# Performance work log

Measured on AMD Instinct MI355X. Metric: run time of the kernel, lower is better.

Reference implementation:

```python
import jax, jax.numpy as jnp
import numpy as np

B, N, C, K, OUT = 4, 10000, 128, 16, 128


def setup_inputs() -> dict:
    key = jax.random.key(0)
    k1, k2, k3, k4 = jax.random.split(key, 4)
    x = jax.random.normal(k1, (B, N, C), dtype=jnp.float32)
    edge_index = jax.random.randint(k2, (2, B, N, K), 0, N)
    # Linear(2C -> OUT), torch convention W: [OUT, 2C]
    W = jax.random.normal(k3, (OUT, 2 * C), dtype=jnp.float32) * 0.05
    b = jax.random.normal(k4, (OUT,), dtype=jnp.float32) * 0.05
    return {"x": x, "edge_index": edge_index, "W": W, "b": b}


def reference(x, edge_index, W, b):
    # x: [B, N, C] -> [B, C, N]
    xt = jnp.swapaxes(x, 1, 2)
    Bs, Cs, Ns = xt.shape
    # batched_index_select: [C, N] gathered by [N, K] -> [C, N, K], vmapped over batch
    gather = jax.vmap(lambda xb, ib: xb[:, ib])
    x_i = gather(xt, edge_index[1])  # [B, C, N, K]
    x_j = gather(xt, edge_index[0])  # [B, C, N, K]
    rel = jnp.max(x_j - x_i, axis=-1)  # max-relative: [B, C, N]
    # interleave channels: [x_0, rel_0, x_1, rel_1, ...] -> [B, 2C, N]
    feat = jnp.stack([xt, rel], axis=2).reshape(Bs, 2 * Cs, Ns)
    feat = jnp.swapaxes(feat, 1, 2)  # [B, N, 2C]
    out = feat @ W.T + b  # Linear(2C -> OUT)
    return jax.nn.relu(out)
```

## Files before the change

### kernel.cpp

```cpp
#include <hip/hip_runtime.h>


#define Bn 4
#define Nn 10000
#define Cn 128
#define Kn 16
#define OUTn 128
#define Mn 16
#define FPAD 8

typedef __attribute__((ext_vector_type(8))) short short8;
typedef __attribute__((ext_vector_type(4))) float floatx4;

__device__ __forceinline__ unsigned short f2bf(float f) {
    union { float f; unsigned u; } v; v.f = f;
    unsigned r = v.u + 0x7fffu + ((v.u >> 16) & 1u);
    return (unsigned short)(r >> 16);
}
__device__ __forceinline__ float bf2f(unsigned short h) {
    union { unsigned u; float f; } v; v.u = ((unsigned)h) << 16;
    return v.f;
}

__global__ __launch_bounds__(256) void prep_kernel(const float* __restrict__ x,
                                                   const float* __restrict__ W,
                                                   unsigned short* __restrict__ xh,
                                                   unsigned short* __restrict__ Wb) {
    int bi = blockIdx.x;
    int t = threadIdx.x;
    if (bi < 16) {
        int tid = bi * 256 + t;
        int lane = tid & 63;
        int step = (tid >> 6) & 7;
        int tile = tid >> 9;
        int o = tile * 16 + (lane & 15);
        int quad = lane >> 4;
        unsigned short v[8];
#pragma unroll
        for (int j = 0; j < 8; ++j) {
            int c2 = step * 32 + quad * 8 + j;
            v[j] = f2bf(W[o * (2 * Cn) + c2]);
        }
        uint4 pk;
        pk.x = (unsigned)v[0] | ((unsigned)v[1] << 16);
        pk.y = (unsigned)v[2] | ((unsigned)v[3] << 16);
        pk.z = (unsigned)v[4] | ((unsigned)v[5] << 16);
        pk.w = (unsigned)v[6] | ((unsigned)v[7] << 16);
        *(uint4*)(Wb + (size_t)tid * 8) = pk;
        return;
    }
    int i = (bi - 16) * 256 + t;
    const float4* x4 = (const float4*)x;
    float4 a = x4[2 * i];
    float4 c = x4[2 * i + 1];
    uint4 pk;
    pk.x = (unsigned)f2bf(a.x) | ((unsigned)f2bf(a.y) << 16);
    pk.y = (unsigned)f2bf(a.z) | ((unsigned)f2bf(a.w) << 16);
    pk.z = (unsigned)f2bf(c.x) | ((unsigned)f2bf(c.y) << 16);
    pk.w = (unsigned)f2bf(c.z) | ((unsigned)f2bf(c.w) << 16);
    *(uint4*)(xh + 8 * (size_t)i) = pk;
}

__global__ __launch_bounds__(256) void mrconv_batch(
    const unsigned short* __restrict__ xh, const int* __restrict__ edge,
    const unsigned short* __restrict__ Wb, const float* __restrict__ bias,
    float* __restrict__ out, int b)
{
    __shared__ unsigned short sfeat[Mn][2 * Cn + FPAD];
    __shared__ int sidx[2][Mn][Kn];

    const int nb = blockIdx.x;
    const int n0 = nb * Mn;
    const int gbase = b * Nn + n0;

    const int t = threadIdx.x;
    const int wv = t >> 6;
    const int lane = t & 63;

    for (int i = t; i < 2 * Mn * Kn; i += 256) {
        int s = i >> 8;
        int m = (i >> 4) & 15;
        int k = i & 15;
        sidx[s][m][k] = __builtin_nontemporal_load(
            &edge[s * (Bn * Nn * Kn) + (gbase + m) * Kn + k]);
    }
    __syncthreads();

    const unsigned short* xbb = xh + (size_t)b * Nn * Cn;

    {
        const int q = lane >> 4;
        const int l16 = lane & 15;
        const int m = wv * 4 + q;
        const int ch = l16 * 8;
        const short8 xs = *(const short8*)(xbb + (n0 + m) * Cn + ch);
        float r[8];
#pragma unroll
        for (int e = 0; e < 8; ++e) r[e] = -3.402823466e+38f;
#pragma unroll
        for (int kc = 0; kc < 2; ++kc) {
            short8 vj[8], vi[8];
#pragma unroll
            for (int u = 0; u < 8; ++u) {
                const int jj = sidx[0][m][kc * 8 + u];
                const int ii = sidx[1][m][kc * 8 + u];
                vj[u] = *(const short8*)(xbb + jj * Cn + ch);
                vi[u] = *(const short8*)(xbb + ii * Cn + ch);
            }
#pragma unroll
            for (int u = 0; u < 8; ++u) {
#pragma unroll
                for (int e = 0; e < 8; ++e) {
                    r[e] = fmaxf(r[e], bf2f((unsigned short)vj[u][e]) -
                                       bf2f((unsigned short)vi[u][e]));
                }
            }
        }
        uint4 pk0, pk1;
        pk0.x = (unsigned short)xs[0] | ((unsigned)f2bf(r[0]) << 16);
        pk0.y = (unsigned short)xs[1] | ((unsigned)f2bf(r[1]) << 16);
        pk0.z = (unsigned short)xs[2] | ((unsigned)f2bf(r[2]) << 16);
        pk0.w = (unsigned short)xs[3] | ((unsigned)f2bf(r[3]) << 16);
        pk1.x = (unsigned short)xs[4] | ((unsigned)f2bf(r[4]) << 16);
        pk1.y = (unsigned short)xs[5] | ((unsigned)f2bf(r[5]) << 16);
        pk1.z = (unsigned short)xs[6] | ((unsigned)f2bf(r[6]) << 16);
        pk1.w = (unsigned short)xs[7] | ((unsigned)f2bf(r[7]) << 16);
        *(uint4*)&sfeat[m][2 * ch] = pk0;
        *(uint4*)&sfeat[m][2 * ch + 8] = pk1;
    }
    __syncthreads();

    const int m16 = lane & 15;
    const int quad = lane >> 4;
    floatx4 acc0 = {0.f, 0.f, 0.f, 0.f};
    floatx4 acc1 = {0.f, 0.f, 0.f, 0.f};
    const short8* wb8 = (const short8*)Wb;
    const int tile0 = 2 * wv, tile1 = 2 * wv + 1;
#pragma unroll
    for (int step = 0; step < 8; ++step) {
        short8 a = *(const short8*)&sfeat[m16][step * 32 + quad * 8];
        short8 b0 = wb8[(tile0 * 8 + step) * 64 + lane];
        short8 b1 = wb8[(tile1 * 8 + step) * 64 + lane];
        acc0 = __builtin_amdgcn_mfma_f32_16x16x32_bf16(a, b0, acc0, 0, 0, 0);
        acc1 = __builtin_amdgcn_mfma_f32_16x16x32_bf16(a, b1, acc1, 0, 0, 0);
    }
    const int o0 = tile0 * 16 + m16;
    const int o1 = tile1 * 16 + m16;
    const float bb0 = bias[o0], bb1 = bias[o1];
#pragma unroll
    for (int r = 0; r < 4; ++r) {
        int g = gbase + quad * 4 + r;
        __builtin_nontemporal_store(fmaxf(acc0[r] + bb0, 0.f), &out[g * OUTn + o0]);
        __builtin_nontemporal_store(fmaxf(acc1[r] + bb1, 0.f), &out[g * OUTn + o1]);
    }
}

extern "C" void kernel_launch(void* const* d_in, const int* in_sizes, int n_in,
                              void* d_out, int out_size, void* d_ws, size_t ws_size,
                              hipStream_t stream) {
    const float* x = (const float*)d_in[0];
    const int* edge = (const int*)d_in[1];
    const float* W = (const float*)d_in[2];
    const float* bias = (const float*)d_in[3];
    float* out = (float*)d_out;

    unsigned short* Wb = (unsigned short*)d_ws;
    unsigned short* xh = (unsigned short*)((char*)d_ws + 65536);

    prep_kernel<<<2516, 256, 0, stream>>>(x, W, xh, Wb);
    for (int b = 0; b < Bn; ++b) {
        mrconv_batch<<<Nn / Mn, 256, 0, stream>>>(xh, edge, Wb, bias, out, b);
    }
}
```

Baseline: 114.8 us.

## Merge per-batch launches into one kernel with XCD-affine dynamic tile scheduling

Replaces four per-batch launches with a single launch whose blocks read their XCC id, pick a batch from it, and claim tiles through atomic counters, stealing from other batches once their own runs out. The aim is to keep each batch's gathered bf16 x rows inside one XCD's L2 for better gather hit rates, and to remove launch gaps and tail effects between batches. It adds a global atomic per block and an inline s_getreg of HW_REG_XCC_ID, and relies on the counters being zeroed by the prep kernel. The grid is 2560 blocks, which exactly covers the 2500 tiles plus a few spares that exit early.

```diff
diff --git a/kernel.cpp b/kernel.cpp
--- a/kernel.cpp
+++ b/kernel.cpp
@@ -7,6 +7,7 @@
 #define Kn 16
 #define OUTn 128
 #define Mn 16
+#define NT (Nn / Mn)
 #define FPAD 8
 
 typedef __attribute__((ext_vector_type(8))) short short8;
@@ -25,10 +26,12 @@
 __global__ __launch_bounds__(256) void prep_kernel(const float* __restrict__ x,
                                                    const float* __restrict__ W,
                                                    unsigned short* __restrict__ xh,
-                                                   unsigned short* __restrict__ Wb) {
+                                                   unsigned short* __restrict__ Wb,
+                                                   int* __restrict__ cnt) {
     int bi = blockIdx.x;
     int t = threadIdx.x;
     if (bi < 16) {
+        if (bi == 0 && t < 8) cnt[t] = 0;
         int tid = bi * 256 + t;
         int lane = tid & 63;
         int step = (tid >> 6) & 7;
@@ -61,19 +64,39 @@
     *(uint4*)(xh + 8 * (size_t)i) = pk;
 }
 
-__global__ __launch_bounds__(256) void mrconv_batch(
+__global__ __launch_bounds__(256) void mrconv_kernel(
     const unsigned short* __restrict__ xh, const int* __restrict__ edge,
     const unsigned short* __restrict__ Wb, const float* __restrict__ bias,
-    float* __restrict__ out, int b)
+    float* __restrict__ out, int* __restrict__ cnt)
 {
     __shared__ unsigned short sfeat[Mn][2 * Cn + FPAD];
     __shared__ int sidx[2][Mn][Kn];
+    __shared__ int s_hdr[2];
 
-    const int nb = blockIdx.x;
+    const int t = threadIdx.x;
+
+    if (t == 0) {
+        unsigned xcc = 0;
+        asm volatile("s_getreg_b32 %0, hwreg(HW_REG_XCC_ID)" : "=s"(xcc));
+        int b = (int)(xcc & 3u);
+        int tile = atomicAdd(&cnt[b], 1);
+        int tries = 0;
+        while (tile >= NT && tries < 3) {
+            b = (b + 1) & 3;
+            tile = atomicAdd(&cnt[b], 1);
+            ++tries;
+        }
+        if (tile >= NT) b = -1;
+        s_hdr[0] = b;
+        s_hdr[1] = tile;
+    }
+    __syncthreads();
+    const int b = s_hdr[0];
+    const int nb = s_hdr[1];
+    if (b < 0) return;
+
     const int n0 = nb * Mn;
     const int gbase = b * Nn + n0;
-
-    const int t = threadIdx.x;
     const int wv = t >> 6;
     const int lane = t & 63;
 
@@ -166,9 +189,8 @@
 
     unsigned short* Wb = (unsigned short*)d_ws;
     unsigned short* xh = (unsigned short*)((char*)d_ws + 65536);
+    int* cnt = (int*)((char*)d_ws + 65536 + 10240000);
 
-    prep_kernel<<<2516, 256, 0, stream>>>(x, W, xh, Wb);
-    for (int b = 0; b < Bn; ++b) {
-        mrconv_batch<<<Nn / Mn, 256, 0, stream>>>(xh, edge, Wb, bias, out, b);
-    }
+    prep_kernel<<<2516, 256, 0, stream>>>(x, W, xh, Wb, cnt);
+    mrconv_kernel<<<2560, 256, 0, stream>>>(xh, edge, Wb, bias, out, cnt);
 }
```

New measurement: 122.0 us. 6.3% more time.
